# Optimization experiments

Hardware: AMD Instinct MI355X
Metric: run time of the kernel (lower is better)

## Reference

```python
import jax, jax.numpy as jnp
import numpy as np

SHAPE = (16, 1, 64, 128, 128)  # volume exactly equals the NCC window [64,128,128]
WIN_SIZE = 64.0 * 128.0 * 128.0


def setup_inputs() -> dict:
    key = jax.random.key(0)
    k1, k2, k3, k4 = jax.random.split(key, 4)
    out = jax.random.uniform(k1, SHAPE, dtype=jnp.float32)
    y_pred = jax.random.uniform(k2, SHAPE, dtype=jnp.float32)
    out_ccl = jax.random.randint(k3, SHAPE, 0, 2, dtype=jnp.int32)
    y_ccl = jax.random.randint(k4, SHAPE, 0, 2, dtype=jnp.int32)
    return {"out": out, "y_pred": y_pred, "out_ccl": out_ccl, "y_ccl": y_ccl}


def reference(out, y_pred, out_ccl, y_ccl):
    I, J = out, y_pred
    # masks at full resolution
    mask_I = jnp.where((out < 0.247) & (out_ccl > 0), 0.0, 1.0).astype(I.dtype)
    mask_J = jnp.where((y_pred < 0.247) & (y_ccl > 0), 0.0, 1.0).astype(J.dtype)

    # conv3d with an all-ones [64,128,128] kernel, stride 1, pad 0 over a
    # 64x128x128 volume == global sum per volume (output spatial dims are 1).
    ax = (2, 3, 4)
    I_sum = jnp.sum(I, axis=ax, keepdims=True)          # [B,1,1,1,1]
    J_sum = jnp.sum(J, axis=ax, keepdims=True)
    I2_sum = jnp.sum(I * I, axis=ax, keepdims=True)
    J2_sum = jnp.sum(J * J, axis=ax, keepdims=True)
    IJ_sum = jnp.sum(I * J, axis=ax, keepdims=True)

    u_I = I_sum / WIN_SIZE
    u_J = J_sum / WIN_SIZE
    cross = IJ_sum - u_J * I_sum - u_I * J_sum + u_I * u_J * WIN_SIZE
    I_var = I2_sum - 2.0 * u_I * I_sum + u_I * u_I * WIN_SIZE
    J_var = J2_sum - 2.0 * u_J * J_sum + u_J * u_J * WIN_SIZE
    cc = cross * cross / (I_var * J_var + 1e-5)         # [B,1,1,1,1]

    # broadcast per-volume cc against full-resolution masks, then mean
    return jnp.mean(-cc * mask_J * mask_I)
```

## Files before the change

### kernel.cpp

```cpp
#include <hip/hip_runtime.h>


#define NB   16
#define VOL  (64 * 128 * 128)
#define BPB  256
#define TPB  256
#define EPT  16
#define NBLK (NB * BPB)

__device__ __forceinline__ double wave_reduce(double v) {
    #pragma unroll
    for (int off = 32; off > 0; off >>= 1) v += __shfl_down(v, off, 64);
    return v;
}

__device__ __forceinline__ float mask_thresh() {
    const float c = 0.247f;
    if ((double)c < 0.247) return __uint_as_float(__float_as_uint(c) + 1u);
    return c;
}

__global__ __launch_bounds__(TPB) void ncc_partial(
    const float* __restrict__ I, const float* __restrict__ J,
    const int* __restrict__ CI, const int* __restrict__ CJ,
    double* __restrict__ part)
{
    const int b = blockIdx.y;
    const size_t base = (size_t)b * VOL + (size_t)blockIdx.x * (TPB * EPT);
    const int tid = threadIdx.x;

    const float4* __restrict__ I4 = reinterpret_cast<const float4*>(I + base);
    const float4* __restrict__ J4 = reinterpret_cast<const float4*>(J + base);
    const int4*   __restrict__ C4 = reinterpret_cast<const int4*>(CI + base);
    const int4*   __restrict__ D4 = reinterpret_cast<const int4*>(CJ + base);

    float4 iv[4]; float4 jv[4]; int4 cv[4]; int4 dv[4];
    #pragma unroll
    for (int k = 0; k < 4; ++k) iv[k] = I4[tid + k * TPB];
    #pragma unroll
    for (int k = 0; k < 4; ++k) jv[k] = J4[tid + k * TPB];
    #pragma unroll
    for (int k = 0; k < 4; ++k) cv[k] = C4[tid + k * TPB];
    #pragma unroll
    for (int k = 0; k < 4; ++k) dv[k] = D4[tid + k * TPB];

    const float TH = mask_thresh();
    float sI = 0.f, sJ = 0.f, sI2 = 0.f, sJ2 = 0.f, sIJ = 0.f;
    int cnt = 0;

    #pragma unroll
    for (int k = 0; k < 4; ++k) {
        float fi[4] = {iv[k].x, iv[k].y, iv[k].z, iv[k].w};
        float fj[4] = {jv[k].x, jv[k].y, jv[k].z, jv[k].w};
        int   ki[4] = {cv[k].x, cv[k].y, cv[k].z, cv[k].w};
        int   kj[4] = {dv[k].x, dv[k].y, dv[k].z, dv[k].w};
        #pragma unroll
        for (int e = 0; e < 4; ++e) {
            sI += fi[e];
            sJ += fj[e];
            sI2 = fmaf(fi[e], fi[e], sI2);
            sJ2 = fmaf(fj[e], fj[e], sJ2);
            sIJ = fmaf(fi[e], fj[e], sIJ);
            bool zI = (fi[e] < TH) && (ki[e] > 0);
            bool zJ = (fj[e] < TH) && (kj[e] > 0);
            cnt += (!zI && !zJ) ? 1 : 0;
        }
    }

    double v[6] = {(double)sI, (double)sJ, (double)sI2,
                   (double)sJ2, (double)sIJ, (double)cnt};
    #pragma unroll
    for (int q = 0; q < 6; ++q) v[q] = wave_reduce(v[q]);

    __shared__ double sh[TPB / 64][6];
    const int wave = tid >> 6, lane = tid & 63;
    if (lane == 0) {
        #pragma unroll
        for (int q = 0; q < 6; ++q) sh[wave][q] = v[q];
    }
    __syncthreads();

    if (tid == 0) {
        const int gb = b * BPB + blockIdx.x;
        #pragma unroll
        for (int q = 0; q < 6; ++q) {
            double o = 0.0;
            for (int w = 0; w < TPB / 64; ++w) o += sh[w][q];
            part[(size_t)q * NBLK + gb] = o;
        }
    }
}

__global__ __launch_bounds__(1024) void ncc_final(
    const double* __restrict__ part, float* __restrict__ outp)
{
    const int tid = threadIdx.x;
    const int w = tid >> 6;
    const int l = tid & 63;

    double v[6] = {0, 0, 0, 0, 0, 0};
    #pragma unroll
    for (int k = 0; k < BPB / 64; ++k) {
        const int p = w * BPB + k * 64 + l;
        #pragma unroll
        for (int q = 0; q < 6; ++q) v[q] += part[(size_t)q * NBLK + p];
    }
    #pragma unroll
    for (int q = 0; q < 6; ++q) v[q] = wave_reduce(v[q]);

    __shared__ double acc[NB];
    if (l == 0) {
        const double W = (double)VOL;
        double uI = v[0] / W, uJ = v[1] / W;
        double cross = v[4] - uJ * v[0] - uI * v[1] + uI * uJ * W;
        double Ivar  = v[2] - 2.0 * uI * v[0] + uI * uI * W;
        double Jvar  = v[3] - 2.0 * uJ * v[1] + uJ * uJ * W;
        double cc = (cross * cross) / (Ivar * Jvar + 1e-5);
        acc[w] = -cc * v[5];
    }
    __syncthreads();

    if (tid == 0) {
        double t = 0.0;
        for (int b = 0; b < NB; ++b) t += acc[b];
        outp[0] = (float)(t / ((double)NB * (double)VOL));
    }
}

extern "C" void kernel_launch(void* const* d_in, const int* in_sizes, int n_in,
                              void* d_out, int out_size, void* d_ws, size_t ws_size,
                              hipStream_t stream)
{
    const float* I  = (const float*)d_in[0];
    const float* J  = (const float*)d_in[1];
    const int*   CI = (const int*)d_in[2];
    const int*   CJ = (const int*)d_in[3];
    double* part = (double*)d_ws;

    dim3 grid(BPB, NB);
    ncc_partial<<<grid, TPB, 0, stream>>>(I, J, CI, CJ, part);
    ncc_final<<<1, 1024, 0, stream>>>(part, (float*)d_out);
}
```

Baseline: 240.4 us.

## Give each thread more work with double-buffered register prefetch

Cuts the partial-reduction grid from 256 to 64 blocks per batch, so each thread now processes 16 float4 quads per input instead of 4. Loads are double-buffered in registers, fetching quad i+2 while quad i is processed, to keep loads in flight and reduce per-block reduction overhead. The final kernel now reads a single partial per lane, since there are now exactly 64 blocks per batch. The trade-off is fewer blocks (1024 in total) and only two quads in flight per thread instead of four, which may leave less memory-level parallelism for a bandwidth-bound stream.

```diff
diff --git a/kernel.cpp b/kernel.cpp
--- a/kernel.cpp
+++ b/kernel.cpp
@@ -3,9 +3,9 @@
 
 #define NB   16
 #define VOL  (64 * 128 * 128)
-#define BPB  256
+#define BPB  64
 #define TPB  256
-#define EPT  16
+#define QPT  16
 #define NBLK (NB * BPB)
 
 __device__ __forceinline__ double wave_reduce(double v) {
@@ -25,35 +25,45 @@
     const int* __restrict__ CI, const int* __restrict__ CJ,
     double* __restrict__ part)
 {
-    const int b = blockIdx.y;
-    const size_t base = (size_t)b * VOL + (size_t)blockIdx.x * (TPB * EPT);
+    const int b   = blockIdx.y;
     const int tid = threadIdx.x;
+    const size_t qbase = (size_t)b * (VOL / 4) + (size_t)blockIdx.x * (TPB * QPT) + tid;
 
-    const float4* __restrict__ I4 = reinterpret_cast<const float4*>(I + base);
-    const float4* __restrict__ J4 = reinterpret_cast<const float4*>(J + base);
-    const int4*   __restrict__ C4 = reinterpret_cast<const int4*>(CI + base);
-    const int4*   __restrict__ D4 = reinterpret_cast<const int4*>(CJ + base);
-
-    float4 iv[4]; float4 jv[4]; int4 cv[4]; int4 dv[4];
-    #pragma unroll
-    for (int k = 0; k < 4; ++k) iv[k] = I4[tid + k * TPB];
-    #pragma unroll
-    for (int k = 0; k < 4; ++k) jv[k] = J4[tid + k * TPB];
-    #pragma unroll
-    for (int k = 0; k < 4; ++k) cv[k] = C4[tid + k * TPB];
-    #pragma unroll
-    for (int k = 0; k < 4; ++k) dv[k] = D4[tid + k * TPB];
+    const float4* __restrict__ I4 = reinterpret_cast<const float4*>(I) + qbase;
+    const float4* __restrict__ J4 = reinterpret_cast<const float4*>(J) + qbase;
+    const int4*   __restrict__ C4 = reinterpret_cast<const int4*>(CI) + qbase;
+    const int4*   __restrict__ D4 = reinterpret_cast<const int4*>(CJ) + qbase;
 
     const float TH = mask_thresh();
     float sI = 0.f, sJ = 0.f, sI2 = 0.f, sJ2 = 0.f, sIJ = 0.f;
     int cnt = 0;
 
+    float4 ibuf[2], jbuf[2];
+    int4   cbuf[2], dbuf[2];
+    ibuf[0] = I4[0];        jbuf[0] = J4[0];
+    cbuf[0] = C4[0];        dbuf[0] = D4[0];
+    ibuf[1] = I4[TPB];      jbuf[1] = J4[TPB];
+    cbuf[1] = C4[TPB];      dbuf[1] = D4[TPB];
+
     #pragma unroll
-    for (int k = 0; k < 4; ++k) {
-        float fi[4] = {iv[k].x, iv[k].y, iv[k].z, iv[k].w};
-        float fj[4] = {jv[k].x, jv[k].y, jv[k].z, jv[k].w};
-        int   ki[4] = {cv[k].x, cv[k].y, cv[k].z, cv[k].w};
-        int   kj[4] = {dv[k].x, dv[k].y, dv[k].z, dv[k].w};
+    for (int i = 0; i < QPT; ++i) {
+        const int cur = i & 1;
+        float4 iv = ibuf[cur];
+        float4 jv = jbuf[cur];
+        int4   cv = cbuf[cur];
+        int4   dv = dbuf[cur];
+
+        if (i + 2 < QPT) {
+            ibuf[cur] = I4[(size_t)(i + 2) * TPB];
+            jbuf[cur] = J4[(size_t)(i + 2) * TPB];
+            cbuf[cur] = C4[(size_t)(i + 2) * TPB];
+            dbuf[cur] = D4[(size_t)(i + 2) * TPB];
+        }
+
+        float fi[4] = {iv.x, iv.y, iv.z, iv.w};
+        float fj[4] = {jv.x, jv.y, jv.z, jv.w};
+        int   ki[4] = {cv.x, cv.y, cv.z, cv.w};
+        int   kj[4] = {dv.x, dv.y, dv.z, dv.w};
         #pragma unroll
         for (int e = 0; e < 4; ++e) {
             sI += fi[e];
@@ -98,13 +108,9 @@
     const int w = tid >> 6;
     const int l = tid & 63;
 
-    double v[6] = {0, 0, 0, 0, 0, 0};
+    double v[6];
     #pragma unroll
-    for (int k = 0; k < BPB / 64; ++k) {
-        const int p = w * BPB + k * 64 + l;
-        #pragma unroll
-        for (int q = 0; q < 6; ++q) v[q] += part[(size_t)q * NBLK + p];
-    }
+    for (int q = 0; q < 6; ++q) v[q] = part[(size_t)q * NBLK + w * BPB + l];
     #pragma unroll
     for (int q = 0; q < 6; ++q) v[q] = wave_reduce(v[q]);
 
```

Result: no change. 245.2 us (+2.0%).

## Stream inputs through per-wave LDS ring with async global_load_lds pipelining

Applied to the files above, without the earlier changes.

Replaces the one-shot load-and-reduce block design with persistent-style waves that each loop over 32 chunks. Loads go through a 4-deep LDS ring filled by global_load_lds, with manual vmcnt waits so the next chunks are in flight while the current one is consumed. Block count drops from 4096 to 512, each wave writes its own partial with no block-level sync, and accumulation moves to per-chunk double adds. The gains depend on deeper memory-level parallelism, at the cost of fewer waves in flight and fragile hand-written waitcnt ordering.

```diff
diff --git a/kernel.cpp b/kernel.cpp
--- a/kernel.cpp
+++ b/kernel.cpp
@@ -1,15 +1,20 @@
 #include <hip/hip_runtime.h>
+#include <stdint.h>
 
 
-#define NB   16
-#define VOL  (64 * 128 * 128)
-#define BPB  256
-#define TPB  256
-#define EPT  16
-#define NBLK (NB * BPB)
+#define NB    16
+#define VOL   (64 * 128 * 128)
+#define BPB   32
+#define TPB   256
+#define NWV   4
+#define DEP   4
+#define NST   32
+#define NWP   (NB * BPB * NWV)
+
+static_assert((long long)BPB * NWV * NST * 64 * 4 == (long long)VOL, "coverage");
 
 __device__ __forceinline__ double wave_reduce(double v) {
-    #pragma unroll
+#pragma unroll
     for (int off = 32; off > 0; off >>= 1) v += __shfl_down(v, off, 64);
     return v;
 }
@@ -20,74 +25,93 @@
     return c;
 }
 
+__device__ __forceinline__ void gload_lds16(const void* g, void* l) {
+    __builtin_amdgcn_global_load_lds(
+        (const __attribute__((address_space(1))) void*)g,
+        (__attribute__((address_space(3))) void*)l,
+        16, 0, 0);
+}
+
 __global__ __launch_bounds__(TPB) void ncc_partial(
     const float* __restrict__ I, const float* __restrict__ J,
     const int* __restrict__ CI, const int* __restrict__ CJ,
     double* __restrict__ part)
 {
-    const int b = blockIdx.y;
-    const size_t base = (size_t)b * VOL + (size_t)blockIdx.x * (TPB * EPT);
-    const int tid = threadIdx.x;
+    __shared__ float4 stg[NWV][DEP][4][64];
 
-    const float4* __restrict__ I4 = reinterpret_cast<const float4*>(I + base);
-    const float4* __restrict__ J4 = reinterpret_cast<const float4*>(J + base);
-    const int4*   __restrict__ C4 = reinterpret_cast<const int4*>(CI + base);
-    const int4*   __restrict__ D4 = reinterpret_cast<const int4*>(CJ + base);
+    const int b = blockIdx.y, bx = blockIdx.x;
+    const int tid = threadIdx.x, w = tid >> 6, l = tid & 63;
 
-    float4 iv[4]; float4 jv[4]; int4 cv[4]; int4 dv[4];
-    #pragma unroll
-    for (int k = 0; k < 4; ++k) iv[k] = I4[tid + k * TPB];
-    #pragma unroll
-    for (int k = 0; k < 4; ++k) jv[k] = J4[tid + k * TPB];
-    #pragma unroll
-    for (int k = 0; k < 4; ++k) cv[k] = C4[tid + k * TPB];
-    #pragma unroll
-    for (int k = 0; k < 4; ++k) dv[k] = D4[tid + k * TPB];
+    const size_t q0 = (size_t)b * (VOL / 4) + ((size_t)bx * NWV + w) * (NST * 64);
+
+    const float4* gI = reinterpret_cast<const float4*>(I) + q0 + l;
+    const float4* gJ = reinterpret_cast<const float4*>(J) + q0 + l;
+    const int4*   gC = reinterpret_cast<const int4*>(CI) + q0 + l;
+    const int4*   gD = reinterpret_cast<const int4*>(CJ) + q0 + l;
+
+#pragma unroll
+    for (int s = 0; s < DEP; ++s) {
+        gload_lds16(gI + (size_t)s * 64, &stg[w][s][0][0]);
+        gload_lds16(gJ + (size_t)s * 64, &stg[w][s][1][0]);
+        gload_lds16(gC + (size_t)s * 64, &stg[w][s][2][0]);
+        gload_lds16(gD + (size_t)s * 64, &stg[w][s][3][0]);
+    }
 
     const float TH = mask_thresh();
-    float sI = 0.f, sJ = 0.f, sI2 = 0.f, sJ2 = 0.f, sIJ = 0.f;
+    double aI = 0, aJ = 0, aI2 = 0, aJ2 = 0, aIJ = 0;
     int cnt = 0;
 
-    #pragma unroll
-    for (int k = 0; k < 4; ++k) {
-        float fi[4] = {iv[k].x, iv[k].y, iv[k].z, iv[k].w};
-        float fj[4] = {jv[k].x, jv[k].y, jv[k].z, jv[k].w};
-        int   ki[4] = {cv[k].x, cv[k].y, cv[k].z, cv[k].w};
-        int   kj[4] = {dv[k].x, dv[k].y, dv[k].z, dv[k].w};
-        #pragma unroll
-        for (int e = 0; e < 4; ++e) {
-            sI += fi[e];
-            sJ += fj[e];
-            sI2 = fmaf(fi[e], fi[e], sI2);
-            sJ2 = fmaf(fj[e], fj[e], sJ2);
-            sIJ = fmaf(fi[e], fj[e], sIJ);
-            bool zI = (fi[e] < TH) && (ki[e] > 0);
-            bool zJ = (fj[e] < TH) && (kj[e] > 0);
-            cnt += (!zI && !zJ) ? 1 : 0;
+    auto consume = [&](int slot) {
+        float4 iv = stg[w][slot][0][l];
+        float4 jv = stg[w][slot][1][l];
+        int4   cv = *reinterpret_cast<const int4*>(&stg[w][slot][2][l]);
+        int4   dv = *reinterpret_cast<const int4*>(&stg[w][slot][3][l]);
+
+        float pI  = (iv.x + iv.y) + (iv.z + iv.w);
+        float pJ  = (jv.x + jv.y) + (jv.z + jv.w);
+        float pI2 = fmaf(iv.x, iv.x, fmaf(iv.y, iv.y, fmaf(iv.z, iv.z, iv.w * iv.w)));
+        float pJ2 = fmaf(jv.x, jv.x, fmaf(jv.y, jv.y, fmaf(jv.z, jv.z, jv.w * jv.w)));
+        float pIJ = fmaf(iv.x, jv.x, fmaf(iv.y, jv.y, fmaf(iv.z, jv.z, iv.w * jv.w)));
+
+        int pc = 0;
+        {
+            bool zI, zJ;
+            zI = (iv.x < TH) && (cv.x > 0); zJ = (jv.x < TH) && (dv.x > 0); pc += (!zI && !zJ);
+            zI = (iv.y < TH) && (cv.y > 0); zJ = (jv.y < TH) && (dv.y > 0); pc += (!zI && !zJ);
+            zI = (iv.z < TH) && (cv.z > 0); zJ = (jv.z < TH) && (dv.z > 0); pc += (!zI && !zJ);
+            zI = (iv.w < TH) && (cv.w > 0); zJ = (jv.w < TH) && (dv.w > 0); pc += (!zI && !zJ);
         }
+
+        aI += (double)pI; aJ += (double)pJ;
+        aI2 += (double)pI2; aJ2 += (double)pJ2; aIJ += (double)pIJ;
+        cnt += pc;
+    };
+
+#pragma unroll 4
+    for (int t = 0; t < NST - DEP; ++t) {
+        const int slot = t & (DEP - 1);
+        asm volatile("s_waitcnt vmcnt(12)" ::: "memory");
+        consume(slot);
+        asm volatile("s_waitcnt lgkmcnt(0)" ::: "memory");
+        const size_t s2 = (size_t)(t + DEP) * 64;
+        gload_lds16(gI + s2, &stg[w][slot][0][0]);
+        gload_lds16(gJ + s2, &stg[w][slot][1][0]);
+        gload_lds16(gC + s2, &stg[w][slot][2][0]);
+        gload_lds16(gD + s2, &stg[w][slot][3][0]);
     }
 
-    double v[6] = {(double)sI, (double)sJ, (double)sI2,
-                   (double)sJ2, (double)sIJ, (double)cnt};
-    #pragma unroll
+    asm volatile("s_waitcnt vmcnt(0)" ::: "memory");
+#pragma unroll
+    for (int t = NST - DEP; t < NST; ++t) consume(t & (DEP - 1));
+
+    double v[6] = {aI, aJ, aI2, aJ2, aIJ, (double)cnt};
+#pragma unroll
     for (int q = 0; q < 6; ++q) v[q] = wave_reduce(v[q]);
 
-    __shared__ double sh[TPB / 64][6];
-    const int wave = tid >> 6, lane = tid & 63;
-    if (lane == 0) {
-        #pragma unroll
-        for (int q = 0; q < 6; ++q) sh[wave][q] = v[q];
-    }
-    __syncthreads();
-
-    if (tid == 0) {
-        const int gb = b * BPB + blockIdx.x;
-        #pragma unroll
-        for (int q = 0; q < 6; ++q) {
-            double o = 0.0;
-            for (int w = 0; w < TPB / 64; ++w) o += sh[w][q];
-            part[(size_t)q * NBLK + gb] = o;
-        }
+    if (l == 0) {
+        const int gw = (b * BPB + bx) * NWV + w;
+#pragma unroll
+        for (int q = 0; q < 6; ++q) part[(size_t)q * NWP + gw] = v[q];
     }
 }
 
@@ -98,14 +122,13 @@
     const int w = tid >> 6;
     const int l = tid & 63;
 
-    double v[6] = {0, 0, 0, 0, 0, 0};
-    #pragma unroll
-    for (int k = 0; k < BPB / 64; ++k) {
-        const int p = w * BPB + k * 64 + l;
-        #pragma unroll
-        for (int q = 0; q < 6; ++q) v[q] += part[(size_t)q * NBLK + p];
+    double v[6];
+#pragma unroll
+    for (int q = 0; q < 6; ++q) {
+        const size_t base = (size_t)q * NWP + (size_t)w * (BPB * NWV);
+        v[q] = part[base + l] + part[base + 64 + l];
     }
-    #pragma unroll
+#pragma unroll
     for (int q = 0; q < 6; ++q) v[q] = wave_reduce(v[q]);
 
     __shared__ double acc[NB];
```

Result: no change. 242.9 us (+1.0%).

## Halve block count with strided per-iteration loads and per-iteration double accumulation

Applied to the files above, without the earlier changes.

Each block now covers twice as many elements using an 8-iteration loop over grid-strided float4 loads, instead of a single 16-element contiguous chunk per thread. Partial sums per float4 are promoted to double each iteration, and the final kernel reads two partials per lane instead of four. The aim is fewer blocks and more coalesced, interleaved access, at the cost of more double-precision adds per element and possibly less memory-level parallelism per thread if the loads are not hoisted.

```diff
diff --git a/kernel.cpp b/kernel.cpp
--- a/kernel.cpp
+++ b/kernel.cpp
@@ -3,13 +3,15 @@
 
 #define NB   16
 #define VOL  (64 * 128 * 128)
-#define BPB  256
+#define BPB  128
 #define TPB  256
-#define EPT  16
-#define NBLK (NB * BPB)
+#define ITER 8
+#define NPB  (NB * BPB)
+
+static_assert((long long)BPB * TPB * 4 * ITER == (long long)VOL, "coverage");
 
 __device__ __forceinline__ double wave_reduce(double v) {
-    #pragma unroll
+#pragma unroll
     for (int off = 32; off > 0; off >>= 1) v += __shfl_down(v, off, 64);
     return v;
 }
@@ -25,68 +27,68 @@
     const int* __restrict__ CI, const int* __restrict__ CJ,
     double* __restrict__ part)
 {
-    const int b = blockIdx.y;
-    const size_t base = (size_t)b * VOL + (size_t)blockIdx.x * (TPB * EPT);
+    const int b = blockIdx.y, bx = blockIdx.x;
     const int tid = threadIdx.x;
 
-    const float4* __restrict__ I4 = reinterpret_cast<const float4*>(I + base);
-    const float4* __restrict__ J4 = reinterpret_cast<const float4*>(J + base);
-    const int4*   __restrict__ C4 = reinterpret_cast<const int4*>(CI + base);
-    const int4*   __restrict__ D4 = reinterpret_cast<const int4*>(CJ + base);
+    const float4* __restrict__ I4 = reinterpret_cast<const float4*>(I);
+    const float4* __restrict__ J4 = reinterpret_cast<const float4*>(J);
+    const int4*   __restrict__ C4 = reinterpret_cast<const int4*>(CI);
+    const int4*   __restrict__ D4 = reinterpret_cast<const int4*>(CJ);
 
-    float4 iv[4]; float4 jv[4]; int4 cv[4]; int4 dv[4];
-    #pragma unroll
-    for (int k = 0; k < 4; ++k) iv[k] = I4[tid + k * TPB];
-    #pragma unroll
-    for (int k = 0; k < 4; ++k) jv[k] = J4[tid + k * TPB];
-    #pragma unroll
-    for (int k = 0; k < 4; ++k) cv[k] = C4[tid + k * TPB];
-    #pragma unroll
-    for (int k = 0; k < 4; ++k) dv[k] = D4[tid + k * TPB];
+    const size_t batchq = (size_t)b * (VOL / 4);
+    const float TH = mask_thresh();
 
-    const float TH = mask_thresh();
-    float sI = 0.f, sJ = 0.f, sI2 = 0.f, sJ2 = 0.f, sIJ = 0.f;
+    double aI = 0, aJ = 0, aI2 = 0, aJ2 = 0, aIJ = 0;
     int cnt = 0;
 
-    #pragma unroll
-    for (int k = 0; k < 4; ++k) {
-        float fi[4] = {iv[k].x, iv[k].y, iv[k].z, iv[k].w};
-        float fj[4] = {jv[k].x, jv[k].y, jv[k].z, jv[k].w};
-        int   ki[4] = {cv[k].x, cv[k].y, cv[k].z, cv[k].w};
-        int   kj[4] = {dv[k].x, dv[k].y, dv[k].z, dv[k].w};
-        #pragma unroll
-        for (int e = 0; e < 4; ++e) {
-            sI += fi[e];
-            sJ += fj[e];
-            sI2 = fmaf(fi[e], fi[e], sI2);
-            sJ2 = fmaf(fj[e], fj[e], sJ2);
-            sIJ = fmaf(fi[e], fj[e], sIJ);
-            bool zI = (fi[e] < TH) && (ki[e] > 0);
-            bool zJ = (fj[e] < TH) && (kj[e] > 0);
-            cnt += (!zI && !zJ) ? 1 : 0;
-        }
+#pragma unroll
+    for (int it = 0; it < ITER; ++it) {
+        const size_t q = batchq + (size_t)it * (BPB * TPB) + (size_t)bx * TPB + tid;
+        float4 iv = I4[q];
+        float4 jv = J4[q];
+        int4   cv = C4[q];
+        int4   dv = D4[q];
+
+        float pI  = (iv.x + iv.y) + (iv.z + iv.w);
+        float pJ  = (jv.x + jv.y) + (jv.z + jv.w);
+        float pI2 = fmaf(iv.x, iv.x, fmaf(iv.y, iv.y, fmaf(iv.z, iv.z, iv.w * iv.w)));
+        float pJ2 = fmaf(jv.x, jv.x, fmaf(jv.y, jv.y, fmaf(jv.z, jv.z, jv.w * jv.w)));
+        float pIJ = fmaf(iv.x, jv.x, fmaf(iv.y, jv.y, fmaf(iv.z, jv.z, iv.w * jv.w)));
+
+        int pc = 0;
+        bool zI, zJ;
+        zI = (iv.x < TH) && (cv.x > 0); zJ = (jv.x < TH) && (dv.x > 0); pc += (!zI && !zJ);
+        zI = (iv.y < TH) && (cv.y > 0); zJ = (jv.y < TH) && (dv.y > 0); pc += (!zI && !zJ);
+        zI = (iv.z < TH) && (cv.z > 0); zJ = (jv.z < TH) && (dv.z > 0); pc += (!zI && !zJ);
+        zI = (iv.w < TH) && (cv.w > 0); zJ = (jv.w < TH) && (dv.w > 0); pc += (!zI && !zJ);
+
+        aI  += (double)pI;
+        aJ  += (double)pJ;
+        aI2 += (double)pI2;
+        aJ2 += (double)pJ2;
+        aIJ += (double)pIJ;
+        cnt += pc;
     }
 
-    double v[6] = {(double)sI, (double)sJ, (double)sI2,
-                   (double)sJ2, (double)sIJ, (double)cnt};
-    #pragma unroll
+    double v[6] = {aI, aJ, aI2, aJ2, aIJ, (double)cnt};
+#pragma unroll
     for (int q = 0; q < 6; ++q) v[q] = wave_reduce(v[q]);
 
     __shared__ double sh[TPB / 64][6];
     const int wave = tid >> 6, lane = tid & 63;
     if (lane == 0) {
-        #pragma unroll
+#pragma unroll
         for (int q = 0; q < 6; ++q) sh[wave][q] = v[q];
     }
     __syncthreads();
 
     if (tid == 0) {
-        const int gb = b * BPB + blockIdx.x;
-        #pragma unroll
+        const int gb = b * BPB + bx;
+#pragma unroll
         for (int q = 0; q < 6; ++q) {
             double o = 0.0;
             for (int w = 0; w < TPB / 64; ++w) o += sh[w][q];
-            part[(size_t)q * NBLK + gb] = o;
+            part[(size_t)q * NPB + gb] = o;
         }
     }
 }
@@ -98,14 +100,13 @@
     const int w = tid >> 6;
     const int l = tid & 63;
 
-    double v[6] = {0, 0, 0, 0, 0, 0};
-    #pragma unroll
-    for (int k = 0; k < BPB / 64; ++k) {
-        const int p = w * BPB + k * 64 + l;
-        #pragma unroll
-        for (int q = 0; q < 6; ++q) v[q] += part[(size_t)q * NBLK + p];
+    double v[6];
+#pragma unroll
+    for (int q = 0; q < 6; ++q) {
+        const size_t base = (size_t)q * NPB + (size_t)w * BPB;
+        v[q] = part[base + l] + part[base + 64 + l];
     }
-    #pragma unroll
+#pragma unroll
     for (int q = 0; q < 6; ++q) v[q] = wave_reduce(v[q]);
 
     __shared__ double acc[NB];
```

Result: no change. 244.1 us (+1.5%).
